# Kernel tuning notes

Hardware: AMD Instinct MI355X
Metric: run time of the kernel (lower is better)

## Reference

```python
import jax, jax.numpy as jnp
import numpy as np

VOCAB = 10000
EMB = 256
FILTERS = 256
KS = [2, 3, 4]
NUM_LABELS = 6
B, L = 4, 256


def _conv1d_same(x, w, b, k):
    # x: [B, C, L], w: [O, I, k] -> [B, O, L]; torch 'same' pad: left=(k-1)//2
    pad_l = (k - 1) // 2
    pad_r = (k - 1) - pad_l
    y = jax.lax.conv_general_dilated(
        x, w, window_strides=(1,), padding=[(pad_l, pad_r)],
        dimension_numbers=('NCH', 'OIH', 'NCH'))
    return y + b[None, :, None]


def setup_inputs() -> dict:
    key = jax.random.key(0)
    ks = jax.random.split(key, 12)
    s = 0.02
    return {
        'input_ids': jax.random.randint(ks[0], (B, L), 0, VOCAB),
        'emb_table': jax.random.normal(ks[1], (VOCAB, EMB), jnp.float32) * s,
        'w2': jax.random.normal(ks[2], (FILTERS, EMB, 2), jnp.float32) * s,
        'b2': jax.random.normal(ks[3], (FILTERS,), jnp.float32) * s,
        'w3': jax.random.normal(ks[4], (FILTERS, EMB, 3), jnp.float32) * s,
        'b3': jax.random.normal(ks[5], (FILTERS,), jnp.float32) * s,
        'w4': jax.random.normal(ks[6], (FILTERS, EMB, 4), jnp.float32) * s,
        'b4': jax.random.normal(ks[7], (FILTERS,), jnp.float32) * s,
        'triple_w': jax.random.normal(ks[8], (NUM_LABELS, 3 * FILTERS), jnp.float32) * s,
        'triple_b': jax.random.normal(ks[9], (NUM_LABELS,), jnp.float32) * s,
        'score_w': jax.random.normal(ks[10], (1, 3 * FILTERS), jnp.float32) * s,
        'score_b': jax.random.normal(ks[11], (1,), jnp.float32) * s,
    }


def reference(input_ids, emb_table, w2, b2, w3, b3, w4, b4,
              triple_w, triple_b, score_w, score_b):
    emb = emb_table[input_ids]              # [B, L, E]
    x = jnp.transpose(emb, (0, 2, 1))       # [B, E, L]
    outs = [_conv1d_same(x, w, b, k) for (w, b, k)
            in ((w2, b2, 2), (w3, b3, 3), (w4, b4, 4))]
    out = jnp.concatenate(outs, axis=1)     # [B, 3F, L]
    out = jnp.transpose(out, (0, 2, 1))     # [B, L, K], K = 3F
    # dropout is identity in eval mode
    pair = jnp.einsum('bik,bjk->bijk', out, out)          # [B, L, L, K]
    triple_logits = jnp.einsum('bijk,ck->bijc', pair, triple_w) + triple_b
    scores = jnp.einsum('bijk,ck->bijc', pair, score_w) + score_b
    scores = scores[..., 0]                 # squeeze(-1) -> [B, L, L]
    return triple_logits, scores
```

## Files before the change

kernel.cpp:

```cpp
#include <hip/hip_runtime.h>
#include <stdint.h>

#define LSEQ 256
#define EMB  256
#define K3F  768
#define SCOFF (4 * 256 * 256 * 6)

typedef short bf16x8 __attribute__((ext_vector_type(8)));
typedef float f32x4  __attribute__((ext_vector_type(4)));

__device__ __forceinline__ uint16_t f2bf(float x) {
    union { float f; uint32_t u; } c; c.f = x;
    uint32_t r = c.u + 0x7fffu + ((c.u >> 16) & 1u);
    return (uint16_t)(r >> 16);
}

__global__ __launch_bounds__(256) void k_prep(const int* __restrict__ ids,
                                              const float* __restrict__ table,
                                              const float* __restrict__ w2,
                                              const float* __restrict__ w3,
                                              const float* __restrict__ w4,
                                              uint16_t* __restrict__ embB,
                                              uint16_t* __restrict__ Wt2,
                                              uint16_t* __restrict__ Wt3,
                                              uint16_t* __restrict__ Wt4) {
    int blk = blockIdx.x, tid = threadIdx.x;
    if (blk < 32) {
        int b = blk >> 3, l0 = (blk & 7) << 5;
        int r = tid >> 3, p = tid & 7;
        int id = ids[(b << 8) + l0 + r];
        const float* src = table + (size_t)id * EMB + p * 32;
        uint16_t* dst = embB + (size_t)(b * 272 + 4 + l0 + r) * 256 + p * 32;
#pragma unroll
        for (int s = 0; s < 8; ++s) {
            float4 v = *(const float4*)(src + 4 * s);
            uint32_t lo = f2bf(v.x) | ((uint32_t)f2bf(v.y) << 16);
            uint32_t hi = f2bf(v.z) | ((uint32_t)f2bf(v.w) << 16);
            *(uint2*)(dst + 4 * s) = make_uint2(lo, hi);
        }
    } else if (blk < 36) {
        int b = blk - 32;
        int ri = tid >> 4;
        int row = ri < 4 ? ri : 256 + ri;
        int off = (tid & 15) * 16;
        uint16_t* dst = embB + (size_t)(b * 272 + row) * 256 + off;
        *(uint4*)dst = make_uint4(0, 0, 0, 0);
        *(uint4*)(dst + 8) = make_uint4(0, 0, 0, 0);
    } else {
        int n = (blk - 36) * 256 + tid;
        if (n < 65536) {
            int c = n >> 8, i = n & 255;
            float2 v = *(const float2*)(w2 + (c << 9) + (i << 1));
            Wt2[c * 256 + i]         = f2bf(v.x);
            Wt2[65536 + c * 256 + i] = f2bf(v.y);
        } else if (n < 131072) {
            int m = n - 65536;
            int c = m >> 8, i = m & 255;
            const float* s = w3 + c * 768 + i * 3;
#pragma unroll
            for (int t = 0; t < 3; ++t)
                Wt3[t * 65536 + c * 256 + i] = f2bf(s[t]);
        } else {
            int m = n - 131072;
            int c = m >> 8, i = m & 255;
            float4 v = *(const float4*)(w4 + (c << 10) + (i << 2));
            Wt4[c * 256 + i]              = f2bf(v.x);
            Wt4[65536 + c * 256 + i]      = f2bf(v.y);
            Wt4[2 * 65536 + c * 256 + i]  = f2bf(v.z);
            Wt4[3 * 65536 + c * 256 + i]  = f2bf(v.w);
        }
    }
}

template <int K, int PAD>
__device__ __forceinline__ void convg_body(const uint16_t* __restrict__ Wt,
                                           const float* __restrict__ bias,
                                           const uint16_t* __restrict__ embB,
                                           const float* __restrict__ tw,
                                           const float* __restrict__ sw,
                                           uint16_t* __restrict__ VB,
                                           uint16_t* __restrict__ U,
                                           int b, int c0, int l0, int gbase,
                                           uint16_t (*As)[32][72], uint16_t (*Bs)[72],
                                           float (*twb)[32]) {
    const int tid = threadIdx.x;
    {
        int cm = tid >> 5, cc = tid & 31;
        int gch = gbase + c0 + cc;
        float v;
        if (cm < 6) v = tw[cm * K3F + gch];
        else if (cm == 6) v = sw[gch];
        else v = bias[c0 + cc];
        twb[cm][cc] = v;
    }
    const int lane = tid & 63, wave = tid >> 6;
    const int ms = wave >> 1, ns = wave & 1;
    const int m = lane & 15, q = lane >> 4;
    const int ar = tid >> 3, aseg = (tid & 7) * 8;

    f32x4 acc;
#pragma unroll
    for (int z = 0; z < 4; ++z) acc[z] = 0.f;

    for (int i0 = 0; i0 < EMB; i0 += 64) {
        __syncthreads();
#pragma unroll
        for (int t = 0; t < K; ++t) {
            const uint16_t* src = Wt + (size_t)((t * 256 + c0 + ar) * 256 + i0) + aseg;
            *(bf16x8*)&As[t][ar][aseg] = *(const bf16x8*)src;
        }
        {
            const uint16_t* src = embB + (size_t)(b * 272 + 3 + l0 + ar) * 256 + i0 + aseg;
            *(bf16x8*)&Bs[ar][aseg] = *(const bf16x8*)src;
            if (tid < 32) {
                int r2 = 32 + (tid >> 3);
                const uint16_t* s2 = embB + (size_t)(b * 272 + 3 + l0 + r2) * 256 + i0 + aseg;
                *(bf16x8*)&Bs[r2][aseg] = *(const bf16x8*)s2;
            }
        }
        __syncthreads();
#pragma unroll
        for (int t = 0; t < K; ++t) {
#pragma unroll
            for (int kh = 0; kh < 64; kh += 32) {
                bf16x8 afr = *(const bf16x8*)&As[t][ms * 16 + m][kh + q * 8];
                bf16x8 bfr = *(const bf16x8*)&Bs[ns * 16 + m + t - PAD + 1][kh + q * 8];
                acc = __builtin_amdgcn_mfma_f32_16x16x32_bf16(afr, bfr, acc, 0, 0, 0);
            }
        }
    }
    __syncthreads();
    float (*Cs)[36] = (float(*)[36])As;
#pragma unroll
    for (int rg = 0; rg < 4; ++rg)
        Cs[ms * 16 + q * 4 + rg][ns * 16 + m] = acc[rg];
    __syncthreads();
    const int l = tid >> 3, cs = (tid & 7) * 4;
    float vals[4];
#pragma unroll
    for (int v = 0; v < 4; ++v) vals[v] = Cs[cs + v][l] + twb[7][cs + v];
    union { uint16_t h[4]; uint32_t d[2]; } pk;
#pragma unroll
    for (int v = 0; v < 4; ++v) pk.h[v] = f2bf(vals[v]);
    uint16_t* vdst = VB + (size_t)(b * 256 + l0 + l) * K3F + gbase + c0 + cs;
    *(uint2*)vdst = *(const uint2*)pk.d;
#pragma unroll
    for (int cm = 0; cm < 7; ++cm) {
#pragma unroll
        for (int v = 0; v < 4; ++v) pk.h[v] = f2bf(vals[v] * twb[cm][cs + v]);
        uint16_t* udst = U + (size_t)((b * 7 + cm) * 256 + l0 + l) * K3F + gbase + c0 + cs;
        *(uint2*)udst = *(const uint2*)pk.d;
    }
}

__global__ __launch_bounds__(256, 2) void k_convg(const uint16_t* __restrict__ Wt2,
                                                  const uint16_t* __restrict__ Wt3,
                                                  const uint16_t* __restrict__ Wt4,
                                                  const float* __restrict__ b2,
                                                  const float* __restrict__ b3,
                                                  const float* __restrict__ b4,
                                                  const uint16_t* __restrict__ embB,
                                                  const float* __restrict__ tw,
                                                  const float* __restrict__ sw,
                                                  uint16_t* __restrict__ VB,
                                                  uint16_t* __restrict__ U) {
    __shared__ uint16_t As[4][32][72];
    __shared__ uint16_t Bs[36][72];
    __shared__ float twb[8][32];
    int blk = blockIdx.x;
    int b = blk & 3, rest = blk >> 2;
    int g = rest >> 6, rr = rest & 63;
    int c0 = (rr >> 3) * 32, l0 = (rr & 7) * 32;
    if (g == 0)      convg_body<2, 0>(Wt2, b2, embB, tw, sw, VB, U, b, c0, l0, 0,   As, Bs, twb);
    else if (g == 1) convg_body<3, 1>(Wt3, b3, embB, tw, sw, VB, U, b, c0, l0, 256, As, Bs, twb);
    else             convg_body<4, 1>(Wt4, b4, embB, tw, sw, VB, U, b, c0, l0, 512, As, Bs, twb);
}

__global__ __launch_bounds__(256, 4) void k_pairc2(const uint16_t* __restrict__ U,
                                                   const uint16_t* __restrict__ VB,
                                                   const float* __restrict__ tb,
                                                   const float* __restrict__ sb,
                                                   float* __restrict__ dout) {
    __shared__ uint16_t T[96][136];
    int blk = blockIdx.x;
    int b = blk & 3, it = (blk >> 2) & 7;
    int rest = blk >> 5;
    int c = rest % 7, jp = rest / 7;
    int i0 = it * 32, j0 = jp * 64;
    int tid = threadIdx.x;
    int lane = tid & 63, wave = tid >> 6;
    int iw = wave >> 1, jw = wave & 1;
    int m = lane & 15, q = lane >> 4;
    int rr = tid >> 3, seg = (tid & 7) * 16;

    const uint16_t* srcp[3];
    srcp[0] = U + (size_t)((b * 7 + c) * 256 + i0 + rr) * K3F + seg;
    srcp[1] = VB + (size_t)(b * 256 + j0 + rr) * K3F + seg;
    srcp[2] = VB + (size_t)(b * 256 + j0 + 32 + rr) * K3F + seg;

    f32x4 acc[2];
#pragma unroll
    for (int n = 0; n < 2; ++n)
#pragma unroll
        for (int z = 0; z < 4; ++z) acc[n][z] = 0.f;

    for (int kc = 0; kc < K3F; kc += 128) {
        __syncthreads();
#pragma unroll
        for (int p = 0; p < 3; ++p) {
            const uint16_t* s = srcp[p] + kc;
            *(bf16x8*)&T[p * 32 + rr][seg]     = *(const bf16x8*)s;
            *(bf16x8*)&T[p * 32 + rr][seg + 8] = *(const bf16x8*)(s + 8);
        }
        __syncthreads();
#pragma unroll
        for (int kh = 0; kh < 4; ++kh) {
            bf16x8 afr  = *(const bf16x8*)&T[iw * 16 + m][kh * 32 + q * 8];
            bf16x8 bfr0 = *(const bf16x8*)&T[32 + jw * 32 + m][kh * 32 + q * 8];
            bf16x8 bfr1 = *(const bf16x8*)&T[32 + jw * 32 + 16 + m][kh * 32 + q * 8];
            acc[0] = __builtin_amdgcn_mfma_f32_16x16x32_bf16(afr, bfr0, acc[0], 0, 0, 0);
            acc[1] = __builtin_amdgcn_mfma_f32_16x16x32_bf16(afr, bfr1, acc[1], 0, 0, 0);
        }
    }
    float bias = (c < 6) ? tb[c] : sb[0];
#pragma unroll
    for (int n = 0; n < 2; ++n)
#pragma unroll
        for (int rg = 0; rg < 4; ++rg) {
            int i = i0 + iw * 16 + q * 4 + rg;
            int j = j0 + jw * 32 + n * 16 + m;
            float v = acc[n][rg] + bias;
            if (c < 6) dout[((size_t)(b * 256 + i) * 256 + j) * 6 + c] = v;
            else       dout[SCOFF + (size_t)(b * 256 + i) * 256 + j] = v;
        }
}

extern "C" void kernel_launch(void* const* d_in, const int* in_sizes, int n_in,
                              void* d_out, int out_size, void* d_ws, size_t ws_size,
                              hipStream_t stream) {
    const int*   ids   = (const int*)d_in[0];
    const float* table = (const float*)d_in[1];
    const float* w2 = (const float*)d_in[2];
    const float* b2 = (const float*)d_in[3];
    const float* w3 = (const float*)d_in[4];
    const float* b3 = (const float*)d_in[5];
    const float* w4 = (const float*)d_in[6];
    const float* b4 = (const float*)d_in[7];
    const float* tw = (const float*)d_in[8];
    const float* tb = (const float*)d_in[9];
    const float* sw = (const float*)d_in[10];
    const float* sb = (const float*)d_in[11];
    float* dout = (float*)d_out;

    uint8_t* wsb = (uint8_t*)d_ws;
    uint16_t* VB   = (uint16_t*)(wsb + 0);
    uint16_t* U    = (uint16_t*)(wsb + 1572864);
    uint16_t* embB = (uint16_t*)(wsb + 12582912);
    uint16_t* Wt2  = (uint16_t*)(wsb + 13139968);
    uint16_t* Wt3  = (uint16_t*)(wsb + 13402112);
    uint16_t* Wt4  = (uint16_t*)(wsb + 13795328);

    hipLaunchKernelGGL(k_prep,   dim3(804), dim3(256), 0, stream,
                       ids, table, w2, w3, w4, embB, Wt2, Wt3, Wt4);
    hipLaunchKernelGGL(k_convg,  dim3(768), dim3(256), 0, stream,
                       Wt2, Wt3, Wt4, b2, b3, b4, embB, tw, sw, VB, U);
    hipLaunchKernelGGL(k_pairc2, dim3(896), dim3(256), 0, stream, U, VB, tb, sb, dout);
}
```

Baseline: 108.1 us.

## Fuse weight scaling into pair GEMM and drop the precomputed U buffer

The conv kernel no longer writes seven scaled copies of the conv output (U). The pair kernel now loads the per-class weight row into shared memory and scales the I-side tile on the fly before staging it. Both kernels also gain register prefetch of the next K-chunk to overlap global loads with MFMA work, and the conv kernel's occupancy hint rises from 2 to 4 blocks. This removes roughly 10 MB of intermediate writes and reads, at the cost of extra ALU work for bf16 unpack, scale and repack in the pair kernel's load phase.

```diff
diff --git a/kernel.cpp b/kernel.cpp
--- a/kernel.cpp
+++ b/kernel.cpp
@@ -13,6 +13,15 @@
     union { float f; uint32_t u; } c; c.f = x;
     uint32_t r = c.u + 0x7fffu + ((c.u >> 16) & 1u);
     return (uint16_t)(r >> 16);
+}
+
+__device__ __forceinline__ uint32_t scale_pk(uint32_t u, float t0, float t1) {
+    union { uint32_t u; float f; } lo, hi;
+    lo.u = u << 16;
+    hi.u = u & 0xffff0000u;
+    float a = lo.f * t0;
+    float b = hi.f * t1;
+    return (uint32_t)f2bf(a) | ((uint32_t)f2bf(b) << 16);
 }
 
 __global__ __launch_bounds__(256) void k_prep(const int* __restrict__ ids,
@@ -76,49 +85,44 @@
 __device__ __forceinline__ void convg_body(const uint16_t* __restrict__ Wt,
                                            const float* __restrict__ bias,
                                            const uint16_t* __restrict__ embB,
-                                           const float* __restrict__ tw,
-                                           const float* __restrict__ sw,
                                            uint16_t* __restrict__ VB,
-                                           uint16_t* __restrict__ U,
                                            int b, int c0, int l0, int gbase,
-                                           uint16_t (*As)[32][72], uint16_t (*Bs)[72],
-                                           float (*twb)[32]) {
+                                           uint16_t (*As)[32][72], uint16_t (*Bs)[72]) {
     const int tid = threadIdx.x;
-    {
-        int cm = tid >> 5, cc = tid & 31;
-        int gch = gbase + c0 + cc;
-        float v;
-        if (cm < 6) v = tw[cm * K3F + gch];
-        else if (cm == 6) v = sw[gch];
-        else v = bias[c0 + cc];
-        twb[cm][cc] = v;
-    }
     const int lane = tid & 63, wave = tid >> 6;
     const int ms = wave >> 1, ns = wave & 1;
     const int m = lane & 15, q = lane >> 4;
     const int ar = tid >> 3, aseg = (tid & 7) * 8;
 
+    const uint16_t* wsrc  = Wt + (size_t)(c0 + ar) * 256 + aseg;
+    const uint16_t* bsrc  = embB + (size_t)(b * 272 + 3 + l0 + ar) * 256 + aseg;
+    const int r2 = 32 + (tid >> 3);
+    const uint16_t* bsrc2 = embB + (size_t)(b * 272 + 3 + l0 + r2) * 256 + aseg;
+
+    bf16x8 ra[K], rb, rb2;
+#pragma unroll
+    for (int t = 0; t < K; ++t) ra[t] = *(const bf16x8*)(wsrc + t * 65536);
+    rb = *(const bf16x8*)bsrc;
+    if (tid < 32) rb2 = *(const bf16x8*)bsrc2;
+
     f32x4 acc;
 #pragma unroll
     for (int z = 0; z < 4; ++z) acc[z] = 0.f;
 
+#pragma unroll
     for (int i0 = 0; i0 < EMB; i0 += 64) {
         __syncthreads();
 #pragma unroll
-        for (int t = 0; t < K; ++t) {
-            const uint16_t* src = Wt + (size_t)((t * 256 + c0 + ar) * 256 + i0) + aseg;
-            *(bf16x8*)&As[t][ar][aseg] = *(const bf16x8*)src;
-        }
-        {
-            const uint16_t* src = embB + (size_t)(b * 272 + 3 + l0 + ar) * 256 + i0 + aseg;
-            *(bf16x8*)&Bs[ar][aseg] = *(const bf16x8*)src;
-            if (tid < 32) {
-                int r2 = 32 + (tid >> 3);
-                const uint16_t* s2 = embB + (size_t)(b * 272 + 3 + l0 + r2) * 256 + i0 + aseg;
-                *(bf16x8*)&Bs[r2][aseg] = *(const bf16x8*)s2;
-            }
-        }
-        __syncthreads();
+        for (int t = 0; t < K; ++t) *(bf16x8*)&As[t][ar][aseg] = ra[t];
+        *(bf16x8*)&Bs[ar][aseg] = rb;
+        if (tid < 32) *(bf16x8*)&Bs[r2][aseg] = rb2;
+        __syncthreads();
+        if (i0 + 64 < EMB) {
+#pragma unroll
+            for (int t = 0; t < K; ++t) ra[t] = *(const bf16x8*)(wsrc + t * 65536 + i0 + 64);
+            rb = *(const bf16x8*)(bsrc + i0 + 64);
+            if (tid < 32) rb2 = *(const bf16x8*)(bsrc2 + i0 + 64);
+        }
 #pragma unroll
         for (int t = 0; t < K; ++t) {
 #pragma unroll
@@ -136,67 +140,68 @@
         Cs[ms * 16 + q * 4 + rg][ns * 16 + m] = acc[rg];
     __syncthreads();
     const int l = tid >> 3, cs = (tid & 7) * 4;
-    float vals[4];
-#pragma unroll
-    for (int v = 0; v < 4; ++v) vals[v] = Cs[cs + v][l] + twb[7][cs + v];
+    const float4 bv = *(const float4*)(bias + c0 + cs);
     union { uint16_t h[4]; uint32_t d[2]; } pk;
-#pragma unroll
-    for (int v = 0; v < 4; ++v) pk.h[v] = f2bf(vals[v]);
+    pk.h[0] = f2bf(Cs[cs + 0][l] + bv.x);
+    pk.h[1] = f2bf(Cs[cs + 1][l] + bv.y);
+    pk.h[2] = f2bf(Cs[cs + 2][l] + bv.z);
+    pk.h[3] = f2bf(Cs[cs + 3][l] + bv.w);
     uint16_t* vdst = VB + (size_t)(b * 256 + l0 + l) * K3F + gbase + c0 + cs;
-    *(uint2*)vdst = *(const uint2*)pk.d;
-#pragma unroll
-    for (int cm = 0; cm < 7; ++cm) {
-#pragma unroll
-        for (int v = 0; v < 4; ++v) pk.h[v] = f2bf(vals[v] * twb[cm][cs + v]);
-        uint16_t* udst = U + (size_t)((b * 7 + cm) * 256 + l0 + l) * K3F + gbase + c0 + cs;
-        *(uint2*)udst = *(const uint2*)pk.d;
-    }
-}
-
-__global__ __launch_bounds__(256, 2) void k_convg(const uint16_t* __restrict__ Wt2,
+    *(uint2*)vdst = make_uint2(pk.d[0], pk.d[1]);
+}
+
+__global__ __launch_bounds__(256, 4) void k_convg(const uint16_t* __restrict__ Wt2,
                                                   const uint16_t* __restrict__ Wt3,
                                                   const uint16_t* __restrict__ Wt4,
                                                   const float* __restrict__ b2,
                                                   const float* __restrict__ b3,
                                                   const float* __restrict__ b4,
                                                   const uint16_t* __restrict__ embB,
-                                                  const float* __restrict__ tw,
-                                                  const float* __restrict__ sw,
-                                                  uint16_t* __restrict__ VB,
-                                                  uint16_t* __restrict__ U) {
-    __shared__ uint16_t As[4][32][72];
-    __shared__ uint16_t Bs[36][72];
-    __shared__ float twb[8][32];
+                                                  uint16_t* __restrict__ VB) {
+    __shared__ __align__(16) uint16_t As[4][32][72];
+    __shared__ __align__(16) uint16_t Bs[36][72];
     int blk = blockIdx.x;
     int b = blk & 3, rest = blk >> 2;
     int g = rest >> 6, rr = rest & 63;
     int c0 = (rr >> 3) * 32, l0 = (rr & 7) * 32;
-    if (g == 0)      convg_body<2, 0>(Wt2, b2, embB, tw, sw, VB, U, b, c0, l0, 0,   As, Bs, twb);
-    else if (g == 1) convg_body<3, 1>(Wt3, b3, embB, tw, sw, VB, U, b, c0, l0, 256, As, Bs, twb);
-    else             convg_body<4, 1>(Wt4, b4, embB, tw, sw, VB, U, b, c0, l0, 512, As, Bs, twb);
-}
-
-__global__ __launch_bounds__(256, 4) void k_pairc2(const uint16_t* __restrict__ U,
-                                                   const uint16_t* __restrict__ VB,
+    if (g == 0)      convg_body<2, 0>(Wt2, b2, embB, VB, b, c0, l0, 0,   As, Bs);
+    else if (g == 1) convg_body<3, 1>(Wt3, b3, embB, VB, b, c0, l0, 256, As, Bs);
+    else             convg_body<4, 1>(Wt4, b4, embB, VB, b, c0, l0, 512, As, Bs);
+}
+
+__global__ __launch_bounds__(256, 4) void k_pairc2(const uint16_t* __restrict__ VB,
+                                                   const float* __restrict__ tw,
+                                                   const float* __restrict__ sw,
                                                    const float* __restrict__ tb,
                                                    const float* __restrict__ sb,
                                                    float* __restrict__ dout) {
-    __shared__ uint16_t T[96][136];
+    __shared__ __align__(16) uint16_t T[96][136];
+    __shared__ __align__(16) float twL[768];
     int blk = blockIdx.x;
     int b = blk & 3, it = (blk >> 2) & 7;
     int rest = blk >> 5;
     int c = rest % 7, jp = rest / 7;
     int i0 = it * 32, j0 = jp * 64;
     int tid = threadIdx.x;
+
+    const float* srow = (c < 6) ? (tw + c * K3F) : sw;
+    twL[tid]       = srow[tid];
+    twL[256 + tid] = srow[256 + tid];
+    twL[512 + tid] = srow[512 + tid];
+
     int lane = tid & 63, wave = tid >> 6;
     int iw = wave >> 1, jw = wave & 1;
     int m = lane & 15, q = lane >> 4;
     int rr = tid >> 3, seg = (tid & 7) * 16;
 
-    const uint16_t* srcp[3];
-    srcp[0] = U + (size_t)((b * 7 + c) * 256 + i0 + rr) * K3F + seg;
-    srcp[1] = VB + (size_t)(b * 256 + j0 + rr) * K3F + seg;
-    srcp[2] = VB + (size_t)(b * 256 + j0 + 32 + rr) * K3F + seg;
+    const uint16_t* srcI  = VB + (size_t)(b * 256 + i0 + rr) * K3F + seg;
+    const uint16_t* srcJ0 = VB + (size_t)(b * 256 + j0 + rr) * K3F + seg;
+    const uint16_t* srcJ1 = VB + (size_t)(b * 256 + j0 + 32 + rr) * K3F + seg;
+
+    bf16x8 rI0, rI1, rJ00, rJ01, rJ10, rJ11;
+    rI0  = *(const bf16x8*)(srcI);      rI1  = *(const bf16x8*)(srcI + 8);
+    rJ00 = *(const bf16x8*)(srcJ0);     rJ01 = *(const bf16x8*)(srcJ0 + 8);
+    rJ10 = *(const bf16x8*)(srcJ1);     rJ11 = *(const bf16x8*)(srcJ1 + 8);
 
     f32x4 acc[2];
 #pragma unroll
@@ -204,15 +209,41 @@
 #pragma unroll
         for (int z = 0; z < 4; ++z) acc[n][z] = 0.f;
 
+#pragma unroll
     for (int kc = 0; kc < K3F; kc += 128) {
         __syncthreads();
-#pragma unroll
-        for (int p = 0; p < 3; ++p) {
-            const uint16_t* s = srcp[p] + kc;
-            *(bf16x8*)&T[p * 32 + rr][seg]     = *(const bf16x8*)s;
-            *(bf16x8*)&T[p * 32 + rr][seg + 8] = *(const bf16x8*)(s + 8);
-        }
-        __syncthreads();
+        {
+            const float* twp = twL + kc + seg;
+            float4 t0 = *(const float4*)(twp + 0);
+            float4 t1 = *(const float4*)(twp + 4);
+            float4 t2 = *(const float4*)(twp + 8);
+            float4 t3 = *(const float4*)(twp + 12);
+            union { bf16x8 v; uint32_t u[4]; } a0, a1, r0, r1;
+            a0.v = rI0; a1.v = rI1;
+            r0.u[0] = scale_pk(a0.u[0], t0.x, t0.y);
+            r0.u[1] = scale_pk(a0.u[1], t0.z, t0.w);
+            r0.u[2] = scale_pk(a0.u[2], t1.x, t1.y);
+            r0.u[3] = scale_pk(a0.u[3], t1.z, t1.w);
+            r1.u[0] = scale_pk(a1.u[0], t2.x, t2.y);
+            r1.u[1] = scale_pk(a1.u[1], t2.z, t2.w);
+            r1.u[2] = scale_pk(a1.u[2], t3.x, t3.y);
+            r1.u[3] = scale_pk(a1.u[3], t3.z, t3.w);
+            *(bf16x8*)&T[rr][seg]     = r0.v;
+            *(bf16x8*)&T[rr][seg + 8] = r1.v;
+        }
+        *(bf16x8*)&T[32 + rr][seg]     = rJ00;
+        *(bf16x8*)&T[32 + rr][seg + 8] = rJ01;
+        *(bf16x8*)&T[64 + rr][seg]     = rJ10;
+        *(bf16x8*)&T[64 + rr][seg + 8] = rJ11;
+        __syncthreads();
+        if (kc + 128 < K3F) {
+            rI0  = *(const bf16x8*)(srcI + kc + 128);
+            rI1  = *(const bf16x8*)(srcI + kc + 136);
+            rJ00 = *(const bf16x8*)(srcJ0 + kc + 128);
+            rJ01 = *(const bf16x8*)(srcJ0 + kc + 136);
+            rJ10 = *(const bf16x8*)(srcJ1 + kc + 128);
+            rJ11 = *(const bf16x8*)(srcJ1 + kc + 136);
+        }
 #pragma unroll
         for (int kh = 0; kh < 4; ++kh) {
             bf16x8 afr  = *(const bf16x8*)&T[iw * 16 + m][kh * 32 + q * 8];
@@ -254,15 +285,15 @@
 
     uint8_t* wsb = (uint8_t*)d_ws;
     uint16_t* VB   = (uint16_t*)(wsb + 0);
-    uint16_t* U    = (uint16_t*)(wsb + 1572864);
-    uint16_t* embB = (uint16_t*)(wsb + 12582912);
-    uint16_t* Wt2  = (uint16_t*)(wsb + 13139968);
-    uint16_t* Wt3  = (uint16_t*)(wsb + 13402112);
-    uint16_t* Wt4  = (uint16_t*)(wsb + 13795328);
+    uint16_t* embB = (uint16_t*)(wsb + 1572864);
+    uint16_t* Wt2  = (uint16_t*)(wsb + 2129920);
+    uint16_t* Wt3  = (uint16_t*)(wsb + 2392064);
+    uint16_t* Wt4  = (uint16_t*)(wsb + 2785280);
 
     hipLaunchKernelGGL(k_prep,   dim3(804), dim3(256), 0, stream,
                        ids, table, w2, w3, w4, embB, Wt2, Wt3, Wt4);
     hipLaunchKernelGGL(k_convg,  dim3(768), dim3(256), 0, stream,
-                       Wt2, Wt3, Wt4, b2, b3, b4, embB, tw, sw, VB, U);
-    hipLaunchKernelGGL(k_pairc2, dim3(896), dim3(256), 0, stream, U, VB, tb, sb, dout);
-}
+                       Wt2, Wt3, Wt4, b2, b3, b4, embB, VB);
+    hipLaunchKernelGGL(k_pairc2, dim3(896), dim3(256), 0, stream,
+                       VB, tw, sw, tb, sb, dout);
+}
```

Result: no change. 106.8 us (-1.2%).
